# Performance work log

Hardware: AMD Instinct MI355X
Metric: run time of the kernel (lower is better)

The kernel has to match this reference:

```python
import jax, jax.numpy as jnp
import numpy as np

D_MODEL = 1024
NUM_HEADS = 16
D_K = D_MODEL // NUM_HEADS
THETA = 10000.0
SEQ = 2048
BATCH = 2


def _rope(t, positions):
    # t: [b, h, s, d_k]; positions: [s]
    half = D_K // 2
    freqs = 1.0 / (THETA ** (jnp.arange(0, D_K, 2, dtype=jnp.float32) / D_K))  # [half]
    angles = positions.astype(jnp.float32)[:, None] * freqs[None, :]  # [s, half]
    cos = jnp.cos(angles)  # [s, half]
    sin = jnp.sin(angles)
    tr = t.reshape(t.shape[:-1] + (half, 2))  # pairs are (even, odd) interleaved
    x1, x2 = tr[..., 0], tr[..., 1]
    r1 = x1 * cos - x2 * sin
    r2 = x1 * sin + x2 * cos
    return jnp.stack([r1, r2], axis=-1).reshape(t.shape)


def setup_inputs() -> dict:
    key = jax.random.key(0)
    ks = jax.random.split(key, 5)
    std = float(np.sqrt(2.0 / (D_MODEL + D_MODEL)))
    return {
        "x": jax.random.normal(ks[0], (BATCH, SEQ, D_MODEL), dtype=jnp.float32),
        "token_positions": jnp.arange(SEQ, dtype=jnp.int64 if jax.config.jax_enable_x64 else jnp.int32),
        "wq": std * jax.random.normal(ks[1], (D_MODEL, D_MODEL), dtype=jnp.float32),
        "wk": std * jax.random.normal(ks[2], (D_MODEL, D_MODEL), dtype=jnp.float32),
        "wv": std * jax.random.normal(ks[3], (D_MODEL, D_MODEL), dtype=jnp.float32),
        "wo": std * jax.random.normal(ks[4], (D_MODEL, D_MODEL), dtype=jnp.float32),
    }


def reference(x, token_positions, wq, wk, wv, wo):
    b, s, _ = x.shape
    # projections: weight is (d_out, d_in), y = x @ W^T
    def proj(w):
        y = jnp.einsum('bsd,od->bso', x, w)
        return y.reshape(b, s, NUM_HEADS, D_K).transpose(0, 2, 1, 3)  # [b,h,s,dk]
    Q, K, V = proj(wq), proj(wk), proj(wv)
    Q = _rope(Q, token_positions)
    K = _rope(K, token_positions)
    scale = 1.0 / jnp.sqrt(jnp.asarray(D_K, dtype=x.dtype))
    scores = jnp.einsum('bhqd,bhkd->bhqk', Q, K) * scale  # [b,h,s,s]
    causal = jnp.tril(jnp.ones((s, s), dtype=bool))
    scores = jnp.where(causal, scores, jnp.asarray(-jnp.inf, dtype=scores.dtype))
    attn = jax.nn.softmax(scores, axis=-1)
    out = jnp.einsum('bhqk,bhkd->bhqd', attn, V)  # [b,h,s,dk]
    out = out.transpose(0, 2, 1, 3).reshape(b, s, D_MODEL)
    return jnp.einsum('bsd,od->bso', out, wo)
```

## Files before the change

kernel.cpp:

```cpp
#include <hip/hip_runtime.h>
#include <hip/hip_bf16.h>
#include <math.h>

#define BATCH  2
#define SEQ    2048
#define DMODEL 1024
#define NHEADS 16
#define DK     64

typedef __hip_bfloat16 bf16;
typedef short s16x8 __attribute__((ext_vector_type(8)));
typedef float f32x4 __attribute__((ext_vector_type(4)));

union P8 { int4 i4; s16x8 v; short s[8]; };

static __device__ __forceinline__ unsigned short f2bu(float f) {
    bf16 h = __float2bfloat16(f);
    return *reinterpret_cast<unsigned short*>(&h);
}
static __device__ __forceinline__ float bu2f(unsigned short u) {
    return __uint_as_float((unsigned int)u << 16);
}

static __device__ __forceinline__ void gll16(const void* g, void* l) {
    __builtin_amdgcn_global_load_lds(
        (const __attribute__((address_space(1))) unsigned int*)g,
        (__attribute__((address_space(3))) unsigned int*)l, 16, 0, 0);
}

__global__ __launch_bounds__(256) void conv_k(
    const float* __restrict__ x, const float* __restrict__ wq,
    const float* __restrict__ wk, const float* __restrict__ wv,
    const float* __restrict__ wo, bf16* __restrict__ dst)
{
    const size_t e0 = ((size_t)blockIdx.x * 256 + threadIdx.x) << 3;
    const float* src;
    bf16* d;
    if (e0 < (size_t)4194304) { src = x + e0; d = dst + e0; }
    else {
        const size_t r = e0 - 4194304;
        const int wsel = (int)(r >> 20);
        const size_t off = r & 1048575;
        src = (wsel == 0 ? wq : wsel == 1 ? wk : wsel == 2 ? wv : wo) + off;
        d = dst + 4194304 + ((size_t)wsel << 20) + off;
    }
    const float4 a = *(const float4*)src;
    const float4 b = *(const float4*)(src + 4);
    P8 p;
    p.s[0] = (short)f2bu(a.x); p.s[1] = (short)f2bu(a.y);
    p.s[2] = (short)f2bu(a.z); p.s[3] = (short)f2bu(a.w);
    p.s[4] = (short)f2bu(b.x); p.s[5] = (short)f2bu(b.y);
    p.s[6] = (short)f2bu(b.z); p.s[7] = (short)f2bu(b.w);
    *(int4*)d = p.i4;
}

template<int KIND>
__global__ __launch_bounds__(256) void gemm_k(
    const bf16* __restrict__ Ab, const bf16* __restrict__ Wb,
    bf16* __restrict__ O0, bf16* __restrict__ O1, bf16* __restrict__ O2,
    float* __restrict__ Of)
{
    __shared__ __align__(16) short As[128 * 32];
    __shared__ __align__(16) short Ws[128 * 32];
    const int tid  = threadIdx.x;
    const int w    = tid >> 6;
    const int lane = tid & 63;
    const int ln   = lane & 15;
    const int quad = lane >> 4;
    const int lr   = lane >> 2;
    const int lc   = (lane & 3) << 3;
    const int id   = blockIdx.x;
    const int m_base = (id & 31) << 7;
    const int n_base = ((id >> 5) & 7) << 7;
    const int z = id >> 8;
    const bf16* Wz = Wb + ((size_t)z << 20);

    size_t arow0;
    if (KIND == 0) {
        arow0 = (size_t)(m_base + 32 * w + lr) * DMODEL + lc;
    } else {
        const int m = m_base + 32 * w + lr;
        const int b = m >> 11, s = m & (SEQ - 1);
        arow0 = ((size_t)b * NHEADS * SEQ + s) * DK + lc;
    }
    const size_t arow1 = arow0 + (size_t)16 * (KIND == 0 ? DMODEL : DK);
    const size_t wrow0 = (size_t)(n_base + 32 * w + lr) * DMODEL + lc;
    const size_t wrow1 = wrow0 + (size_t)16 * DMODEL;
    short* ldsA0 = &As[1024 * w]; short* ldsA1 = ldsA0 + 512;
    short* ldsW0 = &Ws[1024 * w]; short* ldsW1 = ldsW0 + 512;

    const f32x4 zero4 = {0.f, 0.f, 0.f, 0.f};
    f32x4 acc[4][4];
    #pragma unroll
    for (int i = 0; i < 4; ++i)
        #pragma unroll
        for (int j = 0; j < 4; ++j) acc[i][j] = zero4;

    const int mo = (w >> 1) << 6, no = (w & 1) << 6;

    for (int k0 = 0; k0 < DMODEL; k0 += 32) {
        size_t ka;
        if (KIND == 0) ka = (size_t)k0;
        else           ka = (size_t)(k0 >> 6) * (SEQ * DK) + (k0 & 32);
        __syncthreads();
        gll16(Ab + arow0 + ka, ldsA0);
        gll16(Ab + arow1 + ka, ldsA1);
        gll16(Wz + wrow0 + k0, ldsW0);
        gll16(Wz + wrow1 + k0, ldsW1);
        __syncthreads();
        s16x8 af[4], bw[4];
        #pragma unroll
        for (int i = 0; i < 4; ++i) {
            af[i] = *(const s16x8*)&As[(mo + 16 * i + ln) * 32 + quad * 8];
            bw[i] = *(const s16x8*)&Ws[(no + 16 * i + ln) * 32 + quad * 8];
        }
        #pragma unroll
        for (int mi = 0; mi < 4; ++mi)
            #pragma unroll
            for (int ni = 0; ni < 4; ++ni)
                acc[mi][ni] = __builtin_amdgcn_mfma_f32_16x16x32_bf16(
                    af[mi], bw[ni], acc[mi][ni], 0, 0, 0);
    }

    #pragma unroll
    for (int mi = 0; mi < 4; ++mi) {
        #pragma unroll
        for (int ni = 0; ni < 4; ++ni) {
            const int n = n_base + no + 16 * ni + ln;
            if (KIND == 1) {
                #pragma unroll
                for (int r = 0; r < 4; ++r) {
                    const int m = m_base + mo + 16 * mi + quad * 4 + r;
                    Of[(size_t)m * DMODEL + n] = acc[mi][ni][r];
                }
            } else if (z < 2) {
                bf16* C = (z == 0) ? O0 : O1;
                const int h = n >> 6, d = n & (DK - 1);
                #pragma unroll
                for (int r = 0; r < 4; ++r) {
                    const int m = m_base + mo + 16 * mi + quad * 4 + r;
                    const int b = m >> 11, s = m & (SEQ - 1);
                    C[(((size_t)(b * NHEADS + h) * SEQ) + s) * DK + d] =
                        __float2bfloat16(acc[mi][ni][r]);
                }
            } else {
                const int h = n >> 6, d = n & (DK - 1);
                const int m0v = m_base + mo + 16 * mi + quad * 4;
                const int b = m0v >> 11, s0 = m0v & (SEQ - 1);
                ushort4 pk;
                pk.x = f2bu(acc[mi][ni][0]); pk.y = f2bu(acc[mi][ni][1]);
                pk.z = f2bu(acc[mi][ni][2]); pk.w = f2bu(acc[mi][ni][3]);
                *(ushort4*)(O2 + (((size_t)(b * NHEADS + h) * DK) + d) * SEQ + s0) = pk;
            }
        }
    }
}

__global__ __launch_bounds__(256) void rope_k(bf16* __restrict__ Q, bf16* __restrict__ Kk)
{
    const unsigned int idx = blockIdx.x * 256 + threadIdx.x;
    const unsigned int p = idx & ((1u << 21) - 1);
    const bool isq = (idx >> 21) == 0;
    bf16* buf = isq ? Q : Kk;
    unsigned int* wp = reinterpret_cast<unsigned int*>(buf + ((size_t)p << 1));
    const unsigned int u = *wp;
    const int pi = p & 31;
    const int s = (p >> 5) & (SEQ - 1);
    const float freq = exp2f(-(float)pi * 0.4152410119f);
    float sn, cs;
    sincosf((float)s * freq, &sn, &cs);
    const float e = bu2f((unsigned short)(u & 0xffffu));
    const float o = bu2f((unsigned short)(u >> 16));
    const float sc = isq ? 0.125f : 1.0f;
    const unsigned int lo = f2bu((e * cs - o * sn) * sc);
    const unsigned int hi = f2bu((e * sn + o * cs) * sc);
    *wp = lo | (hi << 16);
}

__global__ __launch_bounds__(256) void attn_k(bf16* __restrict__ Q,
                                              const bf16* __restrict__ Kg,
                                              const bf16* __restrict__ VT)
{
    __shared__ __align__(16) short Ks[64 * 72];
    __shared__ __align__(16) short Vs[64 * 72];
    __shared__ __align__(16) short PT[64 * 72];
    const int tid  = threadIdx.x;
    const int w    = tid >> 6;
    const int lane = tid & 63;
    const int ln   = lane & 15;
    const int quad = lane >> 4;
    const int bh = blockIdx.x & 31;
    const int jt = blockIdx.x >> 5;
    const size_t base = (size_t)bh * (SEQ * DK);
    const int srow = tid >> 2;
    const int sc   = (tid & 3) << 4;
    const int NT = SEQ / 64;

    for (int ph = 0; ph < 2; ++ph) {
        const int qt = ph ? (NT - 1 - jt) : jt;
        const int qrow = qt * 64 + 16 * w + ln;

        P8 qa0, qa1;
        {
            const bf16* qsrc = Q + base + (size_t)qrow * DK + quad * 8;
            qa0.i4 = *(const int4*)(qsrc);
            qa1.i4 = *(const int4*)(qsrc + 32);
        }
        const f32x4 zero4 = {0.f, 0.f, 0.f, 0.f};
        f32x4 o[4];
        #pragma unroll
        for (int mt = 0; mt < 4; ++mt) o[mt] = zero4;
        float lsum = 0.f;

        P8 kk[2], vv[2];
        {
            const bf16* ksrc = Kg + base + (size_t)srow * DK + sc;
            kk[0].i4 = *(const int4*)(ksrc);
            kk[1].i4 = *(const int4*)(ksrc + 8);
            const bf16* vsrc = VT + base + (size_t)srow * SEQ + sc;
            vv[0].i4 = *(const int4*)(vsrc);
            vv[1].i4 = *(const int4*)(vsrc + 8);
        }

        for (int kb = 0; kb <= qt; ++kb) {
            __syncthreads();
            *(s16x8*)&Ks[srow * 72 + sc]     = kk[0].v;
            *(s16x8*)&Ks[srow * 72 + sc + 8] = kk[1].v;
            *(s16x8*)&Vs[srow * 72 + sc]     = vv[0].v;
            *(s16x8*)&Vs[srow * 72 + sc + 8] = vv[1].v;
            __syncthreads();

            if (kb < qt) {
                const bf16* ksrc = Kg + base + (size_t)((kb + 1) * 64 + srow) * DK + sc;
                kk[0].i4 = *(const int4*)(ksrc);
                kk[1].i4 = *(const int4*)(ksrc + 8);
                const bf16* vsrc = VT + base + (size_t)srow * SEQ + (kb + 1) * 64 + sc;
                vv[0].i4 = *(const int4*)(vsrc);
                vv[1].i4 = *(const int4*)(vsrc + 8);
            }

            f32x4 sf[4];
            #pragma unroll
            for (int mt = 0; mt < 4; ++mt) {
                sf[mt] = zero4;
                s16x8 ka  = *(const s16x8*)&Ks[(16 * mt + ln) * 72 + quad * 8];
                s16x8 kb2 = *(const s16x8*)&Ks[(16 * mt + ln) * 72 + 32 + quad * 8];
                sf[mt] = __builtin_amdgcn_mfma_f32_16x16x32_bf16(ka,  qa0.v, sf[mt], 0, 0, 0);
                sf[mt] = __builtin_amdgcn_mfma_f32_16x16x32_bf16(kb2, qa1.v, sf[mt], 0, 0, 0);
            }

            if (kb == qt) {
                #pragma unroll
                for (int mt = 0; mt < 4; ++mt)
                    #pragma unroll
                    for (int r = 0; r < 4; ++r)
                        if (kb * 64 + 16 * mt + quad * 4 + r > qrow) sf[mt][r] = -INFINITY;
            }
            #pragma unroll
            for (int mt = 0; mt < 4; ++mt)
                #pragma unroll
                for (int r = 0; r < 4; ++r) {
                    sf[mt][r] = __expf(sf[mt][r]);
                    lsum += sf[mt][r];
                }

            #pragma unroll
            for (int mt = 0; mt < 4; ++mt) {
                ushort4 pk;
                pk.x = f2bu(sf[mt][0]); pk.y = f2bu(sf[mt][1]);
                pk.z = f2bu(sf[mt][2]); pk.w = f2bu(sf[mt][3]);
                *(ushort4*)&PT[(16 * w + ln) * 72 + 16 * mt + quad * 4] = pk;
            }

            s16x8 pa0 = *(const s16x8*)&PT[(16 * w + ln) * 72 + quad * 8];
            s16x8 pa1 = *(const s16x8*)&PT[(16 * w + ln) * 72 + 32 + quad * 8];
            #pragma unroll
            for (int mt = 0; mt < 4; ++mt) {
                s16x8 va0 = *(const s16x8*)&Vs[(16 * mt + ln) * 72 + quad * 8];
                s16x8 va1 = *(const s16x8*)&Vs[(16 * mt + ln) * 72 + 32 + quad * 8];
                o[mt] = __builtin_amdgcn_mfma_f32_16x16x32_bf16(va0, pa0, o[mt], 0, 0, 0);
                o[mt] = __builtin_amdgcn_mfma_f32_16x16x32_bf16(va1, pa1, o[mt], 0, 0, 0);
            }
        }

        lsum += __shfl_xor(lsum, 16, 64);
        lsum += __shfl_xor(lsum, 32, 64);
        const float inv = 1.0f / lsum;
        #pragma unroll
        for (int mt = 0; mt < 4; ++mt) {
            ushort4 st;
            st.x = f2bu(o[mt][0] * inv); st.y = f2bu(o[mt][1] * inv);
            st.z = f2bu(o[mt][2] * inv); st.w = f2bu(o[mt][3] * inv);
            *(ushort4*)(Q + base + (size_t)qrow * DK + 16 * mt + quad * 4) = st;
        }
    }
}

extern "C" void kernel_launch(void* const* d_in, const int* in_sizes, int n_in,
                              void* d_out, int out_size, void* d_ws, size_t ws_size,
                              hipStream_t stream)
{
    const float* x  = (const float*)d_in[0];
    const float* wq = (const float*)d_in[2];
    const float* wk = (const float*)d_in[3];
    const float* wv = (const float*)d_in[4];
    const float* wo = (const float*)d_in[5];

    bf16* wsb   = (bf16*)d_ws;
    bf16* xb    = wsb;
    bf16* wqkvb = wsb + ((size_t)4 << 20);
    bf16* wob   = wsb + ((size_t)7 << 20);
    bf16* Qw    = wsb + ((size_t)8 << 20);
    bf16* Kw    = wsb + ((size_t)12 << 20);
    bf16* VTw   = wsb + ((size_t)16 << 20);

    conv_k<<<4096, 256, 0, stream>>>(x, wq, wk, wv, wo, wsb);
    gemm_k<0><<<768, 256, 0, stream>>>(xb, wqkvb, Qw, Kw, VTw, nullptr);
    rope_k<<<(BATCH * NHEADS * SEQ * DK / 2) / 256 * 2, 256, 0, stream>>>(Qw, Kw);
    attn_k<<<512, 256, 0, stream>>>(Qw, Kw, VTw);
    gemm_k<1><<<256, 256, 0, stream>>>(Qw, wob, nullptr, nullptr, nullptr, (float*)d_out);
}
```

Baseline: 185.9 us.

## Split attention into one q-tile per block and shrink output GEMM tiles

```diff
diff --git a/kernel.cpp b/kernel.cpp
--- a/kernel.cpp
+++ b/kernel.cpp
@@ -54,11 +54,9 @@
     *(int4*)d = p.i4;
 }
 
-template<int KIND>
-__global__ __launch_bounds__(256) void gemm_k(
+__global__ __launch_bounds__(256) void gemm_qkv(
     const bf16* __restrict__ Ab, const bf16* __restrict__ Wb,
-    bf16* __restrict__ O0, bf16* __restrict__ O1, bf16* __restrict__ O2,
-    float* __restrict__ Of)
+    bf16* __restrict__ O0, bf16* __restrict__ O1, bf16* __restrict__ O2)
 {
     __shared__ __align__(16) short As[128 * 32];
     __shared__ __align__(16) short Ws[128 * 32];
@@ -75,15 +73,8 @@
     const int z = id >> 8;
     const bf16* Wz = Wb + ((size_t)z << 20);
 
-    size_t arow0;
-    if (KIND == 0) {
-        arow0 = (size_t)(m_base + 32 * w + lr) * DMODEL + lc;
-    } else {
-        const int m = m_base + 32 * w + lr;
-        const int b = m >> 11, s = m & (SEQ - 1);
-        arow0 = ((size_t)b * NHEADS * SEQ + s) * DK + lc;
-    }
-    const size_t arow1 = arow0 + (size_t)16 * (KIND == 0 ? DMODEL : DK);
+    const size_t arow0 = (size_t)(m_base + 32 * w + lr) * DMODEL + lc;
+    const size_t arow1 = arow0 + (size_t)16 * DMODEL;
     const size_t wrow0 = (size_t)(n_base + 32 * w + lr) * DMODEL + lc;
     const size_t wrow1 = wrow0 + (size_t)16 * DMODEL;
     short* ldsA0 = &As[1024 * w]; short* ldsA1 = ldsA0 + 512;
@@ -99,12 +90,9 @@
     const int mo = (w >> 1) << 6, no = (w & 1) << 6;
 
     for (int k0 = 0; k0 < DMODEL; k0 += 32) {
-        size_t ka;
-        if (KIND == 0) ka = (size_t)k0;
-        else           ka = (size_t)(k0 >> 6) * (SEQ * DK) + (k0 & 32);
-        __syncthreads();
-        gll16(Ab + arow0 + ka, ldsA0);
-        gll16(Ab + arow1 + ka, ldsA1);
+        __syncthreads();
+        gll16(Ab + arow0 + k0, ldsA0);
+        gll16(Ab + arow1 + k0, ldsA1);
         gll16(Wz + wrow0 + k0, ldsW0);
         gll16(Wz + wrow1 + k0, ldsW1);
         __syncthreads();
@@ -127,15 +115,9 @@
         #pragma unroll
         for (int ni = 0; ni < 4; ++ni) {
             const int n = n_base + no + 16 * ni + ln;
-            if (KIND == 1) {
-                #pragma unroll
-                for (int r = 0; r < 4; ++r) {
-                    const int m = m_base + mo + 16 * mi + quad * 4 + r;
-                    Of[(size_t)m * DMODEL + n] = acc[mi][ni][r];
-                }
-            } else if (z < 2) {
+            const int h = n >> 6, d = n & (DK - 1);
+            if (z < 2) {
                 bf16* C = (z == 0) ? O0 : O1;
-                const int h = n >> 6, d = n & (DK - 1);
                 #pragma unroll
                 for (int r = 0; r < 4; ++r) {
                     const int m = m_base + mo + 16 * mi + quad * 4 + r;
@@ -144,7 +126,6 @@
                         __float2bfloat16(acc[mi][ni][r]);
                 }
             } else {
-                const int h = n >> 6, d = n & (DK - 1);
                 const int m0v = m_base + mo + 16 * mi + quad * 4;
                 const int b = m0v >> 11, s0 = m0v & (SEQ - 1);
                 ushort4 pk;
@@ -154,6 +135,75 @@
             }
         }
     }
+}
+
+__global__ __launch_bounds__(256) void gemm_wo(
+    const bf16* __restrict__ Ab, const bf16* __restrict__ Wb,
+    float* __restrict__ Of)
+{
+    __shared__ __align__(16) short As[64 * 32];
+    __shared__ __align__(16) short Ws[128 * 32];
+    const int tid  = threadIdx.x;
+    const int w    = tid >> 6;
+    const int lane = tid & 63;
+    const int ln   = lane & 15;
+    const int quad = lane >> 4;
+    const int lr   = lane >> 2;
+    const int lc   = (lane & 3) << 3;
+    const int id   = blockIdx.x;
+    const int m_base = (id & 63) << 6;
+    const int n_base = (id >> 6) << 7;
+
+    const int am = m_base + 16 * w + lr;
+    const int ab = am >> 11, asx = am & (SEQ - 1);
+    const size_t arow = ((size_t)ab * NHEADS * SEQ + asx) * DK + lc;
+    const size_t wrow0 = (size_t)(n_base + 32 * w + lr) * DMODEL + lc;
+    const size_t wrow1 = wrow0 + (size_t)16 * DMODEL;
+    short* ldsA0 = &As[512 * w];
+    short* ldsW0 = &Ws[1024 * w]; short* ldsW1 = ldsW0 + 512;
+
+    const f32x4 zero4 = {0.f, 0.f, 0.f, 0.f};
+    f32x4 acc[2][4];
+    #pragma unroll
+    for (int i = 0; i < 2; ++i)
+        #pragma unroll
+        for (int j = 0; j < 4; ++j) acc[i][j] = zero4;
+
+    const int mo = (w >> 1) << 5, no = (w & 1) << 6;
+
+    for (int k0 = 0; k0 < DMODEL; k0 += 32) {
+        const size_t ka = (size_t)(k0 >> 6) * (SEQ * DK) + (k0 & 32);
+        __syncthreads();
+        gll16(Ab + arow + ka, ldsA0);
+        gll16(Wb + wrow0 + k0, ldsW0);
+        gll16(Wb + wrow1 + k0, ldsW1);
+        __syncthreads();
+        s16x8 af[2], bw[4];
+        #pragma unroll
+        for (int i = 0; i < 2; ++i)
+            af[i] = *(const s16x8*)&As[(mo + 16 * i + ln) * 32 + quad * 8];
+        #pragma unroll
+        for (int j = 0; j < 4; ++j)
+            bw[j] = *(const s16x8*)&Ws[(no + 16 * j + ln) * 32 + quad * 8];
+        #pragma unroll
+        for (int mi = 0; mi < 2; ++mi)
+            #pragma unroll
+            for (int ni = 0; ni < 4; ++ni)
+                acc[mi][ni] = __builtin_amdgcn_mfma_f32_16x16x32_bf16(
+                    af[mi], bw[ni], acc[mi][ni], 0, 0, 0);
+    }
+
+    #pragma unroll
+    for (int mi = 0; mi < 2; ++mi)
+        #pragma unroll
+        for (int ni = 0; ni < 4; ++ni) {
+            const int n = n_base + no + 16 * ni + ln;
+            #pragma unroll
+            for (int r = 0; r < 4; ++r) {
+                const int m = m_base + mo + 16 * mi + quad * 4 + r;
+                Of[(size_t)m * DMODEL + n] = acc[mi][ni][r];
+            }
+        }
 }
 
 __global__ __launch_bounds__(256) void rope_k(bf16* __restrict__ Q, bf16* __restrict__ Kk)
@@ -190,109 +240,104 @@
     const int ln   = lane & 15;
     const int quad = lane >> 4;
     const int bh = blockIdx.x & 31;
-    const int jt = blockIdx.x >> 5;
+    const int qt = 31 - (blockIdx.x >> 5);
     const size_t base = (size_t)bh * (SEQ * DK);
     const int srow = tid >> 2;
     const int sc   = (tid & 3) << 4;
-    const int NT = SEQ / 64;
-
-    for (int ph = 0; ph < 2; ++ph) {
-        const int qt = ph ? (NT - 1 - jt) : jt;
-        const int qrow = qt * 64 + 16 * w + ln;
-
-        P8 qa0, qa1;
-        {
-            const bf16* qsrc = Q + base + (size_t)qrow * DK + quad * 8;
-            qa0.i4 = *(const int4*)(qsrc);
-            qa1.i4 = *(const int4*)(qsrc + 32);
-        }
-        const f32x4 zero4 = {0.f, 0.f, 0.f, 0.f};
-        f32x4 o[4];
-        #pragma unroll
-        for (int mt = 0; mt < 4; ++mt) o[mt] = zero4;
-        float lsum = 0.f;
-
-        P8 kk[2], vv[2];
-        {
-            const bf16* ksrc = Kg + base + (size_t)srow * DK + sc;
+    const int qrow = qt * 64 + 16 * w + ln;
+
+    P8 qa0, qa1;
+    {
+        const bf16* qsrc = Q + base + (size_t)qrow * DK + quad * 8;
+        qa0.i4 = *(const int4*)(qsrc);
+        qa1.i4 = *(const int4*)(qsrc + 32);
+    }
+    const f32x4 zero4 = {0.f, 0.f, 0.f, 0.f};
+    f32x4 o[4];
+    #pragma unroll
+    for (int mt = 0; mt < 4; ++mt) o[mt] = zero4;
+    float lsum = 0.f;
+
+    P8 kk[2], vv[2];
+    {
+        const bf16* ksrc = Kg + base + (size_t)srow * DK + sc;
+        kk[0].i4 = *(const int4*)(ksrc);
+        kk[1].i4 = *(const int4*)(ksrc + 8);
+        const bf16* vsrc = VT + base + (size_t)srow * SEQ + sc;
+        vv[0].i4 = *(const int4*)(vsrc);
+        vv[1].i4 = *(const int4*)(vsrc + 8);
+    }
+
+    for (int kb = 0; kb <= qt; ++kb) {
+        __syncthreads();
+        *(s16x8*)&Ks[srow * 72 + sc]     = kk[0].v;
+        *(s16x8*)&Ks[srow * 72 + sc + 8] = kk[1].v;
+        *(s16x8*)&Vs[srow * 72 + sc]     = vv[0].v;
+        *(s16x8*)&Vs[srow * 72 + sc + 8] = vv[1].v;
+        __syncthreads();
+
+        if (kb < qt) {
+            const bf16* ksrc = Kg + base + (size_t)((kb + 1) * 64 + srow) * DK + sc;
             kk[0].i4 = *(const int4*)(ksrc);
             kk[1].i4 = *(const int4*)(ksrc + 8);
-            const bf16* vsrc = VT + base + (size_t)srow * SEQ + sc;
+            const bf16* vsrc = VT + base + (size_t)srow * SEQ + (kb + 1) * 64 + sc;
             vv[0].i4 = *(const int4*)(vsrc);
             vv[1].i4 = *(const int4*)(vsrc + 8);
         }
 
-        for (int kb = 0; kb <= qt; ++kb) {
-            __syncthreads();
-            *(s16x8*)&Ks[srow * 72 + sc]     = kk[0].v;
-            *(s16x8*)&Ks[srow * 72 + sc + 8] = kk[1].v;
-            *(s16x8*)&Vs[srow * 72 + sc]     = vv[0].v;
-            *(s16x8*)&Vs[srow * 72 + sc + 8] = vv[1].v;
-            __syncthreads();
-
-            if (kb < qt) {
-                const bf16* ksrc = Kg + base + (size_t)((kb + 1) * 64 + srow) * DK + sc;
-                kk[0].i4 = *(const int4*)(ksrc);
-                kk[1].i4 = *(const int4*)(ksrc + 8);
-                const bf16* vsrc = VT + base + (size_t)srow * SEQ + (kb + 1) * 64 + sc;
-                vv[0].i4 = *(const int4*)(vsrc);
-                vv[1].i4 = *(const int4*)(vsrc + 8);
-            }
-
-            f32x4 sf[4];
-            #pragma unroll
-            for (int mt = 0; mt < 4; ++mt) {
-                sf[mt] = zero4;
-                s16x8 ka  = *(const s16x8*)&Ks[(16 * mt + ln) * 72 + quad * 8];
-                s16x8 kb2 = *(const s16x8*)&Ks[(16 * mt + ln) * 72 + 32 + quad * 8];
-                sf[mt] = __builtin_amdgcn_mfma_f32_16x16x32_bf16(ka,  qa0.v, sf[mt], 0, 0, 0);
-                sf[mt] = __builtin_amdgcn_mfma_f32_16x16x32_bf16(kb2, qa1.v, sf[mt], 0, 0, 0);
-            }
-
-            if (kb == qt) {
-                #pragma unroll
-                for (int mt = 0; mt < 4; ++mt)
-                    #pragma unroll
-                    for (int r = 0; r < 4; ++r)
-                        if (kb * 64 + 16 * mt + quad * 4 + r > qrow) sf[mt][r] = -INFINITY;
-            }
+        f32x4 sf[4];
+        #pragma unroll
+        for (int mt = 0; mt < 4; ++mt) {
+            sf[mt] = zero4;
+            s16x8 ka  = *(const s16x8*)&Ks[(16 * mt + ln) * 72 + quad * 8];
+            s16x8 kb2 = *(const s16x8*)&Ks[(16 * mt + ln) * 72 + 32 + quad * 8];
+            sf[mt] = __builtin_amdgcn_mfma_f32_16x16x32_bf16(ka,  qa0.v, sf[mt], 0, 0, 0);
+            sf[mt] = __builtin_amdgcn_mfma_f32_16x16x32_bf16(kb2, qa1.v, sf[mt], 0, 0, 0);
+        }
+
+        if (kb == qt) {
             #pragma unroll
             for (int mt = 0; mt < 4; ++mt)
                 #pragma unroll
-                for (int r = 0; r < 4; ++r) {
-                    sf[mt][r] = __expf(sf[mt][r]);
-                    lsum += sf[mt][r];
-                }
-
-            #pragma unroll
-            for (int mt = 0; mt < 4; ++mt) {
-                ushort4 pk;
-                pk.x = f2bu(sf[mt][0]); pk.y = f2bu(sf[mt][1]);
-                pk.z = f2bu(sf[mt][2]); pk.w = f2bu(sf[mt][3]);
-                *(ushort4*)&PT[(16 * w + ln) * 72 + 16 * mt + quad * 4] = pk;
+                for (int r = 0; r < 4; ++r)
+                    if (kb * 64 + 16 * mt + quad * 4 + r > qrow) sf[mt][r] = -INFINITY;
+        }
+        #pragma unroll
+        for (int mt = 0; mt < 4; ++mt)
+            #pragma unroll
+            for (int r = 0; r < 4; ++r) {
+                sf[mt][r] = __expf(sf[mt][r]);
+                lsum += sf[mt][r];
             }
 
-            s16x8 pa0 = *(const s16x8*)&PT[(16 * w + ln) * 72 + quad * 8];
-            s16x8 pa1 = *(const s16x8*)&PT[(16 * w + ln) * 72 + 32 + quad * 8];
-            #pragma unroll
-            for (int mt = 0; mt < 4; ++mt) {
-                s16x8 va0 = *(const s16x8*)&Vs[(16 * mt + ln) * 72 + quad * 8];
-                s16x8 va1 = *(const s16x8*)&Vs[(16 * mt + ln) * 72 + 32 + quad * 8];
-                o[mt] = __builtin_amdgcn_mfma_f32_16x16x32_bf16(va0, pa0, o[mt], 0, 0, 0);
-                o[mt] = __builtin_amdgcn_mfma_f32_16x16x32_bf16(va1, pa1, o[mt], 0, 0, 0);
-            }
-        }
-
-        lsum += __shfl_xor(lsum, 16, 64);
-        lsum += __shfl_xor(lsum, 32, 64);
-        const float inv = 1.0f / lsum;
         #pragma unroll
         for (int mt = 0; mt < 4; ++mt) {
-            ushort4 st;
-            st.x = f2bu(o[mt][0] * inv); st.y = f2bu(o[mt][1] * inv);
-            st.z = f2bu(o[mt][2] * inv); st.w = f2bu(o[mt][3] * inv);
-            *(ushort4*)(Q + base + (size_t)qrow * DK + 16 * mt + quad * 4) = st;
-        }
+            ushort4 pk;
+            pk.x = f2bu(sf[mt][0]); pk.y = f2bu(sf[mt][1]);
+            pk.z = f2bu(sf[mt][2]); pk.w = f2bu(sf[mt][3]);
+            *(ushort4*)&PT[(16 * w + ln) * 72 + 16 * mt + quad * 4] = pk;
+        }
+
+        s16x8 pa0 = *(const s16x8*)&PT[(16 * w + ln) * 72 + quad * 8];
+        s16x8 pa1 = *(const s16x8*)&PT[(16 * w + ln) * 72 + 32 + quad * 8];
+        #pragma unroll
+        for (int mt = 0; mt < 4; ++mt) {
+            s16x8 va0 = *(const s16x8*)&Vs[(16 * mt + ln) * 72 + quad * 8];
+            s16x8 va1 = *(const s16x8*)&Vs[(16 * mt + ln) * 72 + 32 + quad * 8];
+            o[mt] = __builtin_amdgcn_mfma_f32_16x16x32_bf16(va0, pa0, o[mt], 0, 0, 0);
+            o[mt] = __builtin_amdgcn_mfma_f32_16x16x32_bf16(va1, pa1, o[mt], 0, 0, 0);
+        }
+    }
+
+    lsum += __shfl_xor(lsum, 16, 64);
+    lsum += __shfl_xor(lsum, 32, 64);
+    const float inv = 1.0f / lsum;
+    #pragma unroll
+    for (int mt = 0; mt < 4; ++mt) {
+        ushort4 st;
+        st.x = f2bu(o[mt][0] * inv); st.y = f2bu(o[mt][1] * inv);
+        st.z = f2bu(o[mt][2] * inv); st.w = f2bu(o[mt][3] * inv);
+        *(ushort4*)(Q + base + (size_t)qrow * DK + 16 * mt + quad * 4) = st;
     }
 }
 
@@ -315,8 +360,8 @@
     bf16* VTw   = wsb + ((size_t)16 << 20);
 
     conv_k<<<4096, 256, 0, stream>>>(x, wq, wk, wv, wo, wsb);
-    gemm_k<0><<<768, 256, 0, stream>>>(xb, wqkvb, Qw, Kw, VTw, nullptr);
+    gemm_qkv<<<768, 256, 0, stream>>>(xb, wqkvb, Qw, Kw, VTw);
     rope_k<<<(BATCH * NHEADS * SEQ * DK / 2) / 256 * 2, 256, 0, stream>>>(Qw, Kw);
-    attn_k<<<512, 256, 0, stream>>>(Qw, Kw, VTw);
-    gemm_k<1><<<256, 256, 0, stream>>>(Qw, wob, nullptr, nullptr, nullptr, (float*)d_out);
-}
+    attn_k<<<1024, 256, 0, stream>>>(Qw, Kw, VTw);
+    gemm_wo<<<512, 256, 0, stream>>>(Qw, wob, (float*)d_out);
+}
```

New measurement: 181.3 us. 2.5% less time.
